# Kernel tuning notes

Hardware: AMD Instinct MI355X
Metric: run time of the kernel (lower is better)

Reference implementation:

```python
import jax, jax.numpy as jnp
from jax import lax
import numpy as np

WINDOW_SIZE = 11
K1 = 0.01
K2 = 0.03
EPS = 1e-06


def _box_filter(x, k):
    """Depthwise uniform box filter with SAME (zero) padding, matching F.conv2d(..., groups=C)."""
    c = x.shape[1]
    kernel = jnp.full((c, 1, k, k), 1.0 / (k * k), dtype=x.dtype)  # [C,1,k,k]
    pad = k // 2
    return lax.conv_general_dilated(
        x, kernel,
        window_strides=(1, 1),
        padding=[(pad, pad), (pad, pad)],
        dimension_numbers=("NCHW", "OIHW", "NCHW"),
        feature_group_count=c,
    )


def setup_inputs() -> dict:
    key = jax.random.key(0)
    k1, k2 = jax.random.split(key)
    shape = (32, 3, 512, 512)
    pred = jax.random.uniform(k1, shape, dtype=jnp.float32)
    target = jax.random.uniform(k2, shape, dtype=jnp.float32)
    return {"pred": pred, "target": target}


def reference(pred, target):
    k = WINDOW_SIZE
    mu_p = _box_filter(pred, k)
    mu_t = _box_filter(target, k)
    sigma_p = _box_filter(pred * pred, k) - mu_p * mu_p
    sigma_t = _box_filter(target * target, k) - mu_t * mu_t
    sigma_x = _box_filter(pred * target, k) - mu_p * mu_t
    sigma_p = jnp.maximum(sigma_p, 0.0)
    sigma_t = jnp.maximum(sigma_t, 0.0)

    # per (batch, channel) dynamic range over spatial dims
    dyn_max = jnp.max(jnp.maximum(pred, target), axis=(-2, -1), keepdims=True)
    dyn_min = jnp.min(jnp.minimum(pred, target), axis=(-2, -1), keepdims=True)
    data_range = jnp.maximum(dyn_max - dyn_min, EPS)
    c1 = (K1 * data_range) ** 2
    c2 = (K2 * data_range) ** 2

    numerator = (2.0 * mu_p * mu_t + c1) * (2.0 * sigma_x + c2)
    denominator = (mu_p * mu_p + mu_t * mu_t + c1) * (sigma_p + sigma_t + c2)
    ssim_map = numerator / (denominator + EPS)
    loss_map = jnp.maximum((1.0 - ssim_map) * 0.5, 0.0)
    return jnp.mean(loss_map)
```

## Files before the change

### kernel.cpp

```cpp
#include <hip/hip_runtime.h>

constexpr int Wd = 512;
constexpr int PLANE = 512 * 512;

__device__ __forceinline__ int swz(int b) { return b ^ ((b >> 3) & 7); }

__global__ __launch_bounds__(256) void minmax_part(const float* __restrict__ pred,
                                                   const float* __restrict__ targ,
                                                   float* __restrict__ pmx,
                                                   float* __restrict__ pmn) {
    int bx = blockIdx.x;
    int plane = bx >> 3, seg = bx & 7;
    size_t base = (size_t)plane * PLANE + (size_t)seg * 32768;
    const float4* p4 = reinterpret_cast<const float4*>(pred + base);
    const float4* t4 = reinterpret_cast<const float4*>(targ + base);
    float mx = -3.0e38f, mn = 3.0e38f;
    for (int i = threadIdx.x; i < 8192; i += 256) {
        float4 a = p4[i], b = t4[i];
        mx = fmaxf(mx, fmaxf(fmaxf(fmaxf(a.x, b.x), fmaxf(a.y, b.y)),
                             fmaxf(fmaxf(a.z, b.z), fmaxf(a.w, b.w))));
        mn = fminf(mn, fminf(fminf(fminf(a.x, b.x), fminf(a.y, b.y)),
                             fminf(fminf(a.z, b.z), fminf(a.w, b.w))));
    }
    #pragma unroll
    for (int off = 32; off; off >>= 1) {
        mx = fmaxf(mx, __shfl_down(mx, off));
        mn = fminf(mn, __shfl_down(mn, off));
    }
    __shared__ float smx[4], smn[4];
    int wid = threadIdx.x >> 6, lane = threadIdx.x & 63;
    if (lane == 0) { smx[wid] = mx; smn[wid] = mn; }
    __syncthreads();
    if (threadIdx.x == 0) {
        pmx[bx] = fmaxf(fmaxf(smx[0], smx[1]), fmaxf(smx[2], smx[3]));
        pmn[bx] = fminf(fminf(smn[0], smn[1]), fminf(smn[2], smn[3]));
    }
}

__global__ void minmax_fin(const float* __restrict__ pmx, const float* __restrict__ pmn,
                           float* __restrict__ c1s, float* __restrict__ c2s, int planes) {
    int p = blockIdx.x * blockDim.x + threadIdx.x;
    if (p < planes) {
        float mx = -3.0e38f, mn = 3.0e38f;
        for (int s = 0; s < 8; ++s) {
            mx = fmaxf(mx, pmx[p * 8 + s]);
            mn = fminf(mn, pmn[p * 8 + s]);
        }
        float dr = fmaxf(mx - mn, 1e-6f);
        float a = 0.01f * dr, b = 0.03f * dr;
        c1s[p] = a * a;
        c2s[p] = b * b;
    }
}

__global__ __launch_bounds__(256) void ssim_main(const float* __restrict__ pred,
                                                 const float* __restrict__ targ,
                                                 const float* __restrict__ c1s,
                                                 const float* __restrict__ c2s,
                                                 float* __restrict__ parts) {
    __shared__ __align__(16) float lds[4 * 5 * 512];
    __shared__ float red[4];
    int bx = blockIdx.x;
    int plane = bx >> 3, tile = bx & 7;
    int wid = threadIdx.x >> 6, c = threadIdx.x & 63;
    const float c1 = c1s[plane], c2 = c2s[plane];
    const float* P = pred + (size_t)plane * PLANE;
    const float* T = targ + (size_t)plane * PLANE;
    float* L = lds + wid * (5 * 512);
    int r0 = tile * 64 + wid * 16;

    float vsP[8], vsT[8], vsPP[8], vsTT[8], vsPT[8];
    #pragma unroll
    for (int k = 0; k < 8; ++k) { vsP[k] = 0; vsT[k] = 0; vsPP[k] = 0; vsTT[k] = 0; vsPT[k] = 0; }

    auto acc = [&](int r, float s) {
        if ((unsigned)r < 512u) {
            const float4* prow = reinterpret_cast<const float4*>(P + (size_t)r * Wd);
            const float4* trow = reinterpret_cast<const float4*>(T + (size_t)r * Wd);
            float4 a0 = prow[2 * c], a1 = prow[2 * c + 1];
            float4 b0 = trow[2 * c], b1 = trow[2 * c + 1];
            float pa[8] = {a0.x, a0.y, a0.z, a0.w, a1.x, a1.y, a1.z, a1.w};
            float tb[8] = {b0.x, b0.y, b0.z, b0.w, b1.x, b1.y, b1.z, b1.w};
            #pragma unroll
            for (int k = 0; k < 8; ++k) {
                float sp = s * pa[k], st = s * tb[k];
                vsP[k]  += sp;
                vsT[k]  += st;
                vsPP[k] += sp * pa[k];
                vsTT[k] += st * tb[k];
                vsPT[k] += sp * tb[k];
            }
        }
    };

    for (int r = r0 - 5; r <= r0 + 4; ++r) acc(r, 1.0f);

    float lsum = 0.0f;
    for (int it = 0; it < 16; ++it) {
        int orow = r0 + it;
        acc(orow + 5, 1.0f);

        float4* L0 = reinterpret_cast<float4*>(L);
        int b0i = swz(2 * c), b1i = swz(2 * c + 1);
        L0[0 * 128 + b0i] = make_float4(vsP[0], vsP[1], vsP[2], vsP[3]);
        L0[0 * 128 + b1i] = make_float4(vsP[4], vsP[5], vsP[6], vsP[7]);
        L0[1 * 128 + b0i] = make_float4(vsT[0], vsT[1], vsT[2], vsT[3]);
        L0[1 * 128 + b1i] = make_float4(vsT[4], vsT[5], vsT[6], vsT[7]);
        L0[2 * 128 + b0i] = make_float4(vsPP[0], vsPP[1], vsPP[2], vsPP[3]);
        L0[2 * 128 + b1i] = make_float4(vsPP[4], vsPP[5], vsPP[6], vsPP[7]);
        L0[3 * 128 + b0i] = make_float4(vsTT[0], vsTT[1], vsTT[2], vsTT[3]);
        L0[3 * 128 + b1i] = make_float4(vsTT[4], vsTT[5], vsTT[6], vsTT[7]);
        L0[4 * 128 + b0i] = make_float4(vsPT[0], vsPT[1], vsPT[2], vsPT[3]);
        L0[4 * 128 + b1i] = make_float4(vsPT[4], vsPT[5], vsPT[6], vsPT[7]);
        __syncthreads();

        float Hq[5][8];
        #pragma unroll
        for (int q = 0; q < 5; ++q) {
            const float4* Lq = reinterpret_cast<const float4*>(L) + q * 128;
            float f[24];
            #pragma unroll
            for (int j = 0; j < 6; ++j) {
                int B = 2 * c - 2 + j;
                int Bc = B < 0 ? 0 : (B > 127 ? 127 : B);
                float4 v = Lq[swz(Bc)];
                if ((unsigned)B > 127u) { v.x = 0; v.y = 0; v.z = 0; v.w = 0; }
                f[4 * j + 0] = v.x; f[4 * j + 1] = v.y; f[4 * j + 2] = v.z; f[4 * j + 3] = v.w;
            }
            float s = f[3];
            #pragma unroll
            for (int k = 4; k <= 13; ++k) s += f[k];
            Hq[q][0] = s;
            #pragma unroll
            for (int i = 1; i < 8; ++i) { s = s - f[i + 2] + f[i + 13]; Hq[q][i] = s; }
        }

        constexpr float inv = 1.0f / 121.0f;
        #pragma unroll
        for (int i = 0; i < 8; ++i) {
            float mup = Hq[0][i] * inv, mut = Hq[1][i] * inv;
            float spp = fmaxf(Hq[2][i] * inv - mup * mup, 0.0f);
            float stt = fmaxf(Hq[3][i] * inv - mut * mut, 0.0f);
            float spt = Hq[4][i] * inv - mup * mut;
            float num = (2.0f * mup * mut + c1) * (2.0f * spt + c2);
            float den = (mup * mup + mut * mut + c1) * (spp + stt + c2);
            float ssim = __fdividef(num, den + 1e-6f);
            lsum += fmaxf((1.0f - ssim) * 0.5f, 0.0f);
        }
        __syncthreads();
        acc(orow - 5, -1.0f);
    }

    #pragma unroll
    for (int off = 32; off; off >>= 1) lsum += __shfl_down(lsum, off);
    if (c == 0) red[wid] = lsum;
    __syncthreads();
    if (threadIdx.x == 0) parts[bx] = (red[0] + red[1]) + (red[2] + red[3]);
}

__global__ void finish(const float* __restrict__ parts, float* __restrict__ out,
                       int n, float invN) {
    float s = 0.0f;
    for (int i = threadIdx.x; i < n; i += 256) s += parts[i];
    #pragma unroll
    for (int off = 32; off; off >>= 1) s += __shfl_down(s, off);
    __shared__ float sw[4];
    int wid = threadIdx.x >> 6, lane = threadIdx.x & 63;
    if (lane == 0) sw[wid] = s;
    __syncthreads();
    if (threadIdx.x == 0) out[0] = ((sw[0] + sw[1]) + (sw[2] + sw[3])) * invN;
}

extern "C" void kernel_launch(void* const* d_in, const int* in_sizes, int n_in,
                              void* d_out, int out_size, void* d_ws, size_t ws_size,
                              hipStream_t stream) {
    const float* pred = (const float*)d_in[0];
    const float* targ = (const float*)d_in[1];
    float* out = (float*)d_out;
    int planes = in_sizes[0] / PLANE;
    int G = planes * 8;

    float* ws   = (float*)d_ws;
    float* pmx  = ws;
    float* pmn  = ws + G;
    float* c1s  = ws + 2 * G;
    float* c2s  = ws + 2 * G + planes;
    float* prts = ws + 2 * G + 2 * planes;

    minmax_part<<<G, 256, 0, stream>>>(pred, targ, pmx, pmn);
    minmax_fin<<<(planes + 127) / 128, 128, 0, stream>>>(pmx, pmn, c1s, c2s, planes);
    ssim_main<<<G, 256, 0, stream>>>(pred, targ, c1s, c2s, prts);
    float invN = 1.0f / ((float)planes * (float)PLANE);
    finish<<<1, 256, 0, stream>>>(prts, out, G, invN);
}
```

Measured before the change: 119.8 us.

## Replace LDS horizontal box sum with wavefront shuffle prefix sums

The horizontal 11-wide sum of the vertical column sums no longer goes through LDS. Each lane now builds prefix sums over its 8 columns and exchanges neighbour prefixes with __shfl_up/__shfl_down. This removes the LDS stores, the 30 LDS reads per iteration and both __syncthreads per row. The cost is 11 cross-lane shuffles per quantity and more register pressure, and the main loop is marked unroll 1.

```diff
diff --git a/kernel.cpp b/kernel.cpp
--- a/kernel.cpp
+++ b/kernel.cpp
@@ -2,8 +2,6 @@
 
 constexpr int Wd = 512;
 constexpr int PLANE = 512 * 512;
-
-__device__ __forceinline__ int swz(int b) { return b ^ ((b >> 3) & 7); }
 
 __global__ __launch_bounds__(256) void minmax_part(const float* __restrict__ pred,
                                                    const float* __restrict__ targ,
@@ -58,16 +56,15 @@
                                                  const float* __restrict__ c1s,
                                                  const float* __restrict__ c2s,
                                                  float* __restrict__ parts) {
-    __shared__ __align__(16) float lds[4 * 5 * 512];
     __shared__ float red[4];
     int bx = blockIdx.x;
     int plane = bx >> 3, tile = bx & 7;
     int wid = threadIdx.x >> 6, c = threadIdx.x & 63;
     const float c1 = c1s[plane], c2 = c2s[plane];
-    const float* P = pred + (size_t)plane * PLANE;
-    const float* T = targ + (size_t)plane * PLANE;
-    float* L = lds + wid * (5 * 512);
+    const float* Pg = pred + (size_t)plane * PLANE;
+    const float* Tg = targ + (size_t)plane * PLANE;
     int r0 = tile * 64 + wid * 16;
+    const bool lane0 = (c == 0), lane63 = (c == 63);
 
     float vsP[8], vsT[8], vsPP[8], vsTT[8], vsPT[8];
     #pragma unroll
@@ -75,8 +72,8 @@
 
     auto acc = [&](int r, float s) {
         if ((unsigned)r < 512u) {
-            const float4* prow = reinterpret_cast<const float4*>(P + (size_t)r * Wd);
-            const float4* trow = reinterpret_cast<const float4*>(T + (size_t)r * Wd);
+            const float4* prow = reinterpret_cast<const float4*>(Pg + (size_t)r * Wd);
+            const float4* trow = reinterpret_cast<const float4*>(Tg + (size_t)r * Wd);
             float4 a0 = prow[2 * c], a1 = prow[2 * c + 1];
             float4 b0 = trow[2 * c], b1 = trow[2 * c + 1];
             float pa[8] = {a0.x, a0.y, a0.z, a0.w, a1.x, a1.y, a1.z, a1.w};
@@ -93,61 +90,62 @@
         }
     };
 
+    auto hsum = [&](const float v[8], float H[8]) {
+        float P[8];
+        P[0] = v[0];
+        #pragma unroll
+        for (int k = 1; k < 8; ++k) P[k] = P[k - 1] + v[k];
+        float T = P[7];
+        float Tm  = __shfl_up(T, 1);
+        float Pm2 = __shfl_up(P[2], 1);
+        float Pm3 = __shfl_up(P[3], 1);
+        float Pm4 = __shfl_up(P[4], 1);
+        float Pm5 = __shfl_up(P[5], 1);
+        float Pm6 = __shfl_up(P[6], 1);
+        if (lane0) { Tm = 0; Pm2 = 0; Pm3 = 0; Pm4 = 0; Pm5 = 0; Pm6 = 0; }
+        float Pp0 = __shfl_down(P[0], 1);
+        float Pp1 = __shfl_down(P[1], 1);
+        float Pp2 = __shfl_down(P[2], 1);
+        float Pp3 = __shfl_down(P[3], 1);
+        float Pp4 = __shfl_down(P[4], 1);
+        if (lane63) { Pp0 = 0; Pp1 = 0; Pp2 = 0; Pp3 = 0; Pp4 = 0; }
+        H[0] = (Tm - Pm2) + P[5];
+        H[1] = (Tm - Pm3) + P[6];
+        H[2] = (Tm - Pm4) + T;
+        H[3] = (Tm - Pm5) + (T + Pp0);
+        H[4] = (Tm - Pm6) + (T + Pp1);
+        H[5] = T + Pp2;
+        H[6] = (T - P[0]) + Pp3;
+        H[7] = (T - P[1]) + Pp4;
+    };
+
     for (int r = r0 - 5; r <= r0 + 4; ++r) acc(r, 1.0f);
 
     float lsum = 0.0f;
+    #pragma unroll 1
     for (int it = 0; it < 16; ++it) {
         int orow = r0 + it;
         acc(orow + 5, 1.0f);
 
-        float4* L0 = reinterpret_cast<float4*>(L);
-        int b0i = swz(2 * c), b1i = swz(2 * c + 1);
-        L0[0 * 128 + b0i] = make_float4(vsP[0], vsP[1], vsP[2], vsP[3]);
-        L0[0 * 128 + b1i] = make_float4(vsP[4], vsP[5], vsP[6], vsP[7]);
-        L0[1 * 128 + b0i] = make_float4(vsT[0], vsT[1], vsT[2], vsT[3]);
-        L0[1 * 128 + b1i] = make_float4(vsT[4], vsT[5], vsT[6], vsT[7]);
-        L0[2 * 128 + b0i] = make_float4(vsPP[0], vsPP[1], vsPP[2], vsPP[3]);
-        L0[2 * 128 + b1i] = make_float4(vsPP[4], vsPP[5], vsPP[6], vsPP[7]);
-        L0[3 * 128 + b0i] = make_float4(vsTT[0], vsTT[1], vsTT[2], vsTT[3]);
-        L0[3 * 128 + b1i] = make_float4(vsTT[4], vsTT[5], vsTT[6], vsTT[7]);
-        L0[4 * 128 + b0i] = make_float4(vsPT[0], vsPT[1], vsPT[2], vsPT[3]);
-        L0[4 * 128 + b1i] = make_float4(vsPT[4], vsPT[5], vsPT[6], vsPT[7]);
-        __syncthreads();
-
-        float Hq[5][8];
-        #pragma unroll
-        for (int q = 0; q < 5; ++q) {
-            const float4* Lq = reinterpret_cast<const float4*>(L) + q * 128;
-            float f[24];
-            #pragma unroll
-            for (int j = 0; j < 6; ++j) {
-                int B = 2 * c - 2 + j;
-                int Bc = B < 0 ? 0 : (B > 127 ? 127 : B);
-                float4 v = Lq[swz(Bc)];
-                if ((unsigned)B > 127u) { v.x = 0; v.y = 0; v.z = 0; v.w = 0; }
-                f[4 * j + 0] = v.x; f[4 * j + 1] = v.y; f[4 * j + 2] = v.z; f[4 * j + 3] = v.w;
-            }
-            float s = f[3];
-            #pragma unroll
-            for (int k = 4; k <= 13; ++k) s += f[k];
-            Hq[q][0] = s;
-            #pragma unroll
-            for (int i = 1; i < 8; ++i) { s = s - f[i + 2] + f[i + 13]; Hq[q][i] = s; }
-        }
+        float H[5][8];
+        hsum(vsP,  H[0]);
+        hsum(vsT,  H[1]);
+        hsum(vsPP, H[2]);
+        hsum(vsTT, H[3]);
+        hsum(vsPT, H[4]);
 
         constexpr float inv = 1.0f / 121.0f;
         #pragma unroll
         for (int i = 0; i < 8; ++i) {
-            float mup = Hq[0][i] * inv, mut = Hq[1][i] * inv;
-            float spp = fmaxf(Hq[2][i] * inv - mup * mup, 0.0f);
-            float stt = fmaxf(Hq[3][i] * inv - mut * mut, 0.0f);
-            float spt = Hq[4][i] * inv - mup * mut;
+            float mup = H[0][i] * inv, mut = H[1][i] * inv;
+            float spp = fmaxf(H[2][i] * inv - mup * mup, 0.0f);
+            float stt = fmaxf(H[3][i] * inv - mut * mut, 0.0f);
+            float spt = H[4][i] * inv - mup * mut;
             float num = (2.0f * mup * mut + c1) * (2.0f * spt + c2);
             float den = (mup * mup + mut * mut + c1) * (spp + stt + c2);
             float ssim = __fdividef(num, den + 1e-6f);
             lsum += fmaxf((1.0f - ssim) * 0.5f, 0.0f);
         }
-        __syncthreads();
         acc(orow - 5, -1.0f);
     }
 
```

Result: no change. 120.7 us (+0.7%).
